# Kernel tuning notes

Measured on AMD Instinct MI355X. Metric: run time of the kernel, lower is better.

## Reference

```python
import jax, jax.numpy as jnp
import numpy as np

VOCAB, EMB, HID, OUT = 10, 32, 64, 10
B, T = 4096, 128

def setup_inputs() -> dict:
    key = jax.random.key(0)
    ks = jax.random.split(key, 8)
    num1 = jax.random.randint(ks[0], (B, T), 0, VOCAB, dtype=jnp.int32)
    num2 = jax.random.randint(ks[1], (B, T), 0, VOCAB, dtype=jnp.int32)
    # Glorot-ish scaled params (values irrelevant for correctness baseline)
    E = jax.random.normal(ks[2], (VOCAB, EMB), jnp.float32) * 0.05
    Wxh = jax.random.normal(ks[3], (2 * EMB, HID), jnp.float32) * (1.0 / np.sqrt(2 * EMB))
    Whh = jax.random.normal(ks[4], (HID, HID), jnp.float32) * (1.0 / np.sqrt(HID))
    b = jax.random.normal(ks[5], (HID,), jnp.float32) * 0.01
    Wd = jax.random.normal(ks[6], (HID, OUT), jnp.float32) * (1.0 / np.sqrt(HID))
    bd = jax.random.normal(ks[7], (OUT,), jnp.float32) * 0.01
    return {"num1": num1, "num2": num2, "E": E, "Wxh": Wxh, "Whh": Whh,
            "b": b, "Wd": Wd, "bd": bd}

def reference(num1, num2, E, Wxh, Whh, b, Wd, bd):
    # Embedding lookup + concat: [B, T, 2*EMB]
    x = jnp.concatenate([E[num1], E[num2]], axis=-1)
    # Precompute input projection for all timesteps (batched GEMM)
    xp = jnp.einsum('bti,ih->bth', x, Wxh) + b  # [B, T, HID]
    h0 = jnp.zeros((x.shape[0], Whh.shape[0]), x.dtype)

    def step(h, xt):  # SimpleRNNCell: h' = tanh(x W_xh + b + h W_hh)
        h = jnp.tanh(xt + h @ Whh)
        return h, h

    _, hs = jax.lax.scan(step, h0, jnp.swapaxes(xp, 0, 1))  # [T, B, HID]
    rnn_out = jnp.swapaxes(hs, 0, 1)  # return_sequences=True -> [B, T, HID]
    logits = rnn_out @ Wd + bd  # [B, T, 10]
    return logits
```

## Files before the change

kernel.cpp:

```cpp
#include <hip/hip_runtime.h>


typedef _Float16 half8 __attribute__((ext_vector_type(8)));
typedef __fp16 fp16x2 __attribute__((ext_vector_type(2)));
typedef float floatx4 __attribute__((ext_vector_type(4)));

#define MFMA16(A, B, C) __builtin_amdgcn_mfma_f32_16x16x32_f16((A), (B), (C), 0, 0, 0)
#define BARRIER() asm volatile("s_waitcnt lgkmcnt(0)\n\ts_barrier" ::: "memory")

#define LUT_DW  17408
#define NP_DW   18432
#define POOL_DW 20512

__global__ __launch_bounds__(512)
void rnn_mfma(const int* __restrict__ num1, const int* __restrict__ num2,
              const float* __restrict__ E, const float* __restrict__ Wxh,
              const float* __restrict__ Whh, const float* __restrict__ bias,
              const float* __restrict__ Wd, const float* __restrict__ bd,
              float* __restrict__ out)
{
    __shared__ __align__(16) int pool[POOL_DW];
    int* lutI  = pool + LUT_DW;
    int* numpk = pool + NP_DW;

    const int tid  = threadIdx.x;
    const int wv   = tid >> 6;
    const bool prod = (wv < 4);
    const int w    = wv & 3;
    const int lane = tid & 63;
    const int c    = lane & 15;
    const int q    = lane >> 4;
    const int qs   = q * 8;
    const int g    = blockIdx.x;

    float* WhhS = (float*)pool;
    float* P1t  = (float*)(pool + 4096);
    float* P2t  = (float*)(pool + 4736);
    float* WdS  = (float*)(pool + 5376);
    for (int i = tid; i < 4096; i += 512) WhhS[i] = Whh[i];
    for (int i = tid; i < 640;  i += 512) WdS[i]  = Wd[i];
    for (int idx = tid; idx < 640; idx += 512) {
        int v = idx >> 6, jj = idx & 63;
        float s1 = bias[jj], s2 = 0.f;
        #pragma unroll
        for (int i = 0; i < 32; ++i) {
            float e = E[v * 32 + i];
            s1 = fmaf(e, Wxh[i * 64 + jj], s1);
            s2 = fmaf(e, Wxh[(32 + i) * 64 + jj], s2);
        }
        P1t[idx] = s1;
        P2t[idx] = s2;
    }
    if (tid < 256) {
        int e = tid;
        #pragma unroll
        for (int j = 0; j < 4; ++j)
            lutI[e * 4 + j] = (((e >> (2 * j)) & 1) ? 0x3C00 : 0)
                            | (((e >> (2 * j + 1)) & 1) ? 0x3C000000 : 0);
    }
    for (int idx = tid; idx < 2080; idx += 512) {
        int m = idx & 15, t = idx >> 4;
        int s = g * 16 + m;
        numpk[t * 16 + m] = (t < 128)
            ? ((1 << num1[s * 128 + t]) | (1 << (num2[s * 128 + t] + 10))) : 0;
    }
    __syncthreads();

    half8 Wint[4], Wdint[4], Pf;
    float bdv = 0.f;
    if (prod) {
        #pragma unroll
        for (int kt = 0; kt < 4; ++kt)
            #pragma unroll
            for (int p = 0; p < 4; ++p) {
                int k = kt * 16 + q * 4 + p;
                float wvv = WhhS[k * 64 + w * 16 + c];
                Wint[kt][2 * p]     = (_Float16)wvv;
                Wint[kt][2 * p + 1] = (_Float16)(wvv * 0.015625f);
            }
        #pragma unroll
        for (int j = 0; j < 8; ++j) {
            int i2 = qs + j;
            float pv = (i2 < 10) ? P1t[i2 * 64 + w * 16 + c]
                     : (i2 < 20) ? P2t[(i2 - 10) * 64 + w * 16 + c] : 0.f;
            Pf[j] = (_Float16)pv;
        }
    } else {
        #pragma unroll
        for (int kt = 0; kt < 4; ++kt)
            #pragma unroll
            for (int p = 0; p < 4; ++p) {
                int k = kt * 16 + q * 4 + p;
                float dv = (c < 10) ? WdS[k * 10 + c] : 0.f;
                Wdint[kt][2 * p]     = (_Float16)dv;
                Wdint[kt][2 * p + 1] = (_Float16)(dv * 0.015625f);
            }
        bdv = (c < 10) ? bd[c] : 0.f;
    }
    __syncthreads();

    for (int i = tid; i < 1088; i += 512) pool[15 * 1088 + i] = 0;
    __syncthreads();

    const int rBase = c * 68 + q * 4;
    const floatx4 zero4 = {0.f, 0.f, 0.f, 0.f};

    if (prod) {
        const int wBase = (q * 4) * 68 + w * 16 + c;

        floatx4 Cxp;
        {
            int mk0 = numpk[c];
            half8 Aoh = *(const half8*)&lutI[((mk0 >> qs) & 0xFF) * 4];
            Cxp = MFMA16(Aoh, Pf, zero4);
        }

        for (int half = 0; half < 16; ++half) {
            const int sb  = (half & 1) * 8;
            const int npo = half * 128 + c;
            #pragma unroll
            for (int i = 0; i < 8; ++i) {
                int mk = numpk[npo + (i + 1) * 16];

                const int spw = sb + i;
                const int spr = (i == 0) ? ((sb ^ 8) + 7) : (sb + i - 1);

                half8 A0 = *(const half8*)&pool[spr * 1088 + rBase];
                half8 A1 = *(const half8*)&pool[spr * 1088 + rBase + 16];
                half8 A2 = *(const half8*)&pool[spr * 1088 + rBase + 32];
                half8 A3 = *(const half8*)&pool[spr * 1088 + rBase + 48];

                floatx4 Ca = MFMA16(A0, Wint[0], Cxp);
                Ca         = MFMA16(A1, Wint[1], Ca);
                floatx4 Cb = MFMA16(A2, Wint[2], zero4);
                Cb         = MFMA16(A3, Wint[3], Cb);

                {
                    int mq = (mk >> qs) & 0xFF;
                    half8 Aoh = *(const half8*)&lutI[mq * 4];
                    Cxp = MFMA16(Aoh, Pf, zero4);
                }

                float hv[4];
                #pragma unroll
                for (int r = 0; r < 4; ++r) {
                    float x  = Ca[r] + Cb[r];
                    float e2 = __builtin_amdgcn_exp2f(x * 2.885390081777927f);
                    hv[r] = 1.f - 2.f * __builtin_amdgcn_rcpf(e2 + 1.f);
                }
                #pragma unroll
                for (int p = 0; p < 2; ++p) {
                    fp16x2 ph = __builtin_amdgcn_cvt_pkrtz(hv[2 * p], hv[2 * p + 1]);
                    float c0 = (float)ph[0];
                    float c1 = (float)ph[1];
                    fp16x2 pl = __builtin_amdgcn_cvt_pkrtz((hv[2 * p] - c0) * 64.f,
                                                           (hv[2 * p + 1] - c1) * 64.f);
                    unsigned phu = __builtin_bit_cast(unsigned, ph);
                    unsigned plu = __builtin_bit_cast(unsigned, pl);
                    unsigned w0 = __builtin_amdgcn_perm(plu, phu, 0x05040100u);
                    unsigned w1 = __builtin_amdgcn_perm(plu, phu, 0x07060302u);
                    pool[spw * 1088 + wBase + (2 * p) * 68]     = (int)w0;
                    pool[spw * 1088 + wBase + (2 * p + 1) * 68] = (int)w1;
                }

                BARRIER();
            }
        }
    } else {
        float* outP[2][4];
        #pragma unroll
        for (int u = 0; u < 2; ++u)
            #pragma unroll
            for (int r = 0; r < 4; ++r)
                outP[u][r] = out + (((g * 16 + q * 4 + r) * 128) + 2 * w + u) * 10 + c;
        const bool cLt10 = (c < 10);

        for (int ph = 0; ph < 16; ++ph) {
            const int sbp = (ph & 1) ? 0 : 8;
            #pragma unroll
            for (int i = 0; i < 8; ++i) {
                if (ph > 0 && (i == w || i == w + 4)) {
                    const int u  = (i == w) ? 0 : 1;
                    const int sl = (sbp + 2 * w + u) * 1088 + rBase;
                    half8 P0 = *(const half8*)&pool[sl];
                    half8 P1 = *(const half8*)&pool[sl + 16];
                    half8 P2 = *(const half8*)&pool[sl + 32];
                    half8 P3 = *(const half8*)&pool[sl + 48];
                    floatx4 Cp = MFMA16(P0, Wdint[0], zero4);
                    Cp         = MFMA16(P1, Wdint[1], Cp);
                    Cp         = MFMA16(P2, Wdint[2], Cp);
                    Cp         = MFMA16(P3, Wdint[3], Cp);
                    if (cLt10) {
                        #pragma unroll
                        for (int r = 0; r < 4; ++r)
                            outP[u][r][0] = Cp[r] + bdv;
                    }
                }
                BARRIER();
            }
            if (ph > 0) {
                #pragma unroll
                for (int u = 0; u < 2; ++u)
                    #pragma unroll
                    for (int r = 0; r < 4; ++r)
                        outP[u][r] += 80;
            }
        }

        #pragma unroll
        for (int u = 0; u < 2; ++u) {
            const int sl = (8 + 2 * w + u) * 1088 + rBase;
            half8 P0 = *(const half8*)&pool[sl];
            half8 P1 = *(const half8*)&pool[sl + 16];
            half8 P2 = *(const half8*)&pool[sl + 32];
            half8 P3 = *(const half8*)&pool[sl + 48];
            floatx4 Cp = MFMA16(P0, Wdint[0], zero4);
            Cp         = MFMA16(P1, Wdint[1], Cp);
            Cp         = MFMA16(P2, Wdint[2], Cp);
            Cp         = MFMA16(P3, Wdint[3], Cp);
            if (cLt10) {
                #pragma unroll
                for (int r = 0; r < 4; ++r)
                    outP[u][r][0] = Cp[r] + bdv;
            }
        }
    }
}

extern "C" void kernel_launch(void* const* d_in, const int* in_sizes, int n_in,
                              void* d_out, int out_size, void* d_ws, size_t ws_size,
                              hipStream_t stream) {
    const int*   num1 = (const int*)d_in[0];
    const int*   num2 = (const int*)d_in[1];
    const float* E    = (const float*)d_in[2];
    const float* Wxh  = (const float*)d_in[3];
    const float* Whh  = (const float*)d_in[4];
    const float* b    = (const float*)d_in[5];
    const float* Wd   = (const float*)d_in[6];
    const float* bd   = (const float*)d_in[7];
    float* out = (float*)d_out;
    rnn_mfma<<<256, 512, 0, stream>>>(num1, num2, E, Wxh, Whh, b, Wd, bd, out);
}
```

Measured before the change: 115.1 us.

## Prepack per-lane token bytes and split recurrence MFMAs into four independent chains

Token masks are repacked into a per-lane layout, four timesteps of one-hot bytes per dword. Each lane then loads three dwords per 8-step chunk instead of issuing one LDS read every step. The four recurrent MFMAs now accumulate into separate registers and are summed with VALU adds, which removes the serial MFMA dependency chain on the critical path. This costs extra shared memory, an extra packing pass (no barrier shown after it), and a few more VALU adds per step.

After: 112.8 us. -2.0%, faster.

```diff
diff --git a/kernel.cpp b/kernel.cpp
--- a/kernel.cpp
+++ b/kernel.cpp
@@ -9,8 +9,9 @@
 #define BARRIER() asm volatile("s_waitcnt lgkmcnt(0)\n\ts_barrier" ::: "memory")
 
 #define LUT_DW  17408
-#define NP_DW   18432
-#define POOL_DW 20512
+#define PKM_DW  18432
+#define POOL_DW 20544
+#define NPS_DW  6528
 
 __global__ __launch_bounds__(512)
 void rnn_mfma(const int* __restrict__ num1, const int* __restrict__ num2,
@@ -21,7 +22,8 @@
 {
     __shared__ __align__(16) int pool[POOL_DW];
     int* lutI  = pool + LUT_DW;
-    int* numpk = pool + NP_DW;
+    int* pkm   = pool + PKM_DW;
+    int* npS   = pool + NPS_DW;
 
     const int tid  = threadIdx.x;
     const int wv   = tid >> 6;
@@ -58,13 +60,26 @@
             lutI[e * 4 + j] = (((e >> (2 * j)) & 1) ? 0x3C00 : 0)
                             | (((e >> (2 * j + 1)) & 1) ? 0x3C000000 : 0);
     }
-    for (int idx = tid; idx < 2080; idx += 512) {
+    for (int idx = tid; idx < 2048; idx += 512) {
         int m = idx & 15, t = idx >> 4;
         int s = g * 16 + m;
-        numpk[t * 16 + m] = (t < 128)
-            ? ((1 << num1[s * 128 + t]) | (1 << (num2[s * 128 + t] + 10))) : 0;
+        npS[t * 16 + m] = (1 << num1[s * 128 + t]) | (1 << (num2[s * 128 + t] + 10));
     }
     __syncthreads();
+
+    for (int idx = tid; idx < 64 * 33; idx += 512) {
+        int l  = idx & 63;
+        int tt = idx >> 6;
+        int lc = l & 15, lqs = (l >> 4) * 8;
+        unsigned dw = 0;
+        #pragma unroll
+        for (int k = 0; k < 4; ++k) {
+            int t = tt * 4 + k;
+            unsigned byte = (t < 128) ? ((unsigned)(npS[t * 16 + lc] >> lqs) & 0xFFu) : 0u;
+            dw |= byte << (8 * k);
+        }
+        pkm[l * 33 + tt] = (int)dw;
+    }
 
     half8 Wint[4], Wdint[4], Pf;
     float bdv = 0.f;
@@ -106,22 +121,23 @@
     const floatx4 zero4 = {0.f, 0.f, 0.f, 0.f};
 
     if (prod) {
-        const int wBase = (q * 4) * 68 + w * 16 + c;
+        const int wBase  = (q * 4) * 68 + w * 16 + c;
+        const int pkBase = lane * 33;
 
         floatx4 Cxp;
         {
-            int mk0 = numpk[c];
-            half8 Aoh = *(const half8*)&lutI[((mk0 >> qs) & 0xFF) * 4];
+            unsigned b0 = (unsigned)pkm[pkBase] & 0xFFu;
+            half8 Aoh = *(const half8*)&lutI[b0 * 4];
             Cxp = MFMA16(Aoh, Pf, zero4);
         }
 
         for (int half = 0; half < 16; ++half) {
-            const int sb  = (half & 1) * 8;
-            const int npo = half * 128 + c;
+            const int sb = (half & 1) * 8;
+            int d0 = pkm[pkBase + 2 * half];
+            int d1 = pkm[pkBase + 2 * half + 1];
+            int d2 = pkm[pkBase + 2 * half + 2];
             #pragma unroll
             for (int i = 0; i < 8; ++i) {
-                int mk = numpk[npo + (i + 1) * 16];
-
                 const int spw = sb + i;
                 const int spr = (i == 0) ? ((sb ^ 8) + 7) : (sb + i - 1);
 
@@ -129,22 +145,21 @@
                 half8 A1 = *(const half8*)&pool[spr * 1088 + rBase + 16];
                 half8 A2 = *(const half8*)&pool[spr * 1088 + rBase + 32];
                 half8 A3 = *(const half8*)&pool[spr * 1088 + rBase + 48];
+                unsigned b = (i < 3) ? (((unsigned)d0 >> (8 * (i + 1))) & 0xFFu)
+                           : (i < 7) ? (((unsigned)d1 >> (8 * (i - 3))) & 0xFFu)
+                                     : ((unsigned)d2 & 0xFFu);
+                half8 Aoh = *(const half8*)&lutI[b * 4];
 
                 floatx4 Ca = MFMA16(A0, Wint[0], Cxp);
-                Ca         = MFMA16(A1, Wint[1], Ca);
-                floatx4 Cb = MFMA16(A2, Wint[2], zero4);
-                Cb         = MFMA16(A3, Wint[3], Cb);
-
-                {
-                    int mq = (mk >> qs) & 0xFF;
-                    half8 Aoh = *(const half8*)&lutI[mq * 4];
-                    Cxp = MFMA16(Aoh, Pf, zero4);
-                }
+                floatx4 Cb = MFMA16(A1, Wint[1], zero4);
+                floatx4 Cc = MFMA16(A2, Wint[2], zero4);
+                floatx4 Cd = MFMA16(A3, Wint[3], zero4);
+                Cxp = MFMA16(Aoh, Pf, zero4);
 
                 float hv[4];
                 #pragma unroll
                 for (int r = 0; r < 4; ++r) {
-                    float x  = Ca[r] + Cb[r];
+                    float x  = (Ca[r] + Cb[r]) + (Cc[r] + Cd[r]);
                     float e2 = __builtin_amdgcn_exp2f(x * 2.885390081777927f);
                     hv[r] = 1.f - 2.f * __builtin_amdgcn_rcpf(e2 + 1.f);
                 }
```
